# Performance work log

Hardware: AMD Instinct MI355X
Metric: run time of the kernel (lower is better)

Reference implementation:

```python
import jax, jax.numpy as jnp
import numpy as np

B, S, P, D, H = 2, 1024, 1024, 2048, 16
HD = D // H  # 128
T = P + S


def setup_inputs() -> dict:
    key = jax.random.key(0)
    ks = jax.random.split(key, 12)
    hidden_state = jax.random.normal(ks[0], (B, S, D), dtype=jnp.float32)
    past_key = jax.random.normal(ks[1], (B, H, P, HD), dtype=jnp.float32)
    past_value = jax.random.normal(ks[2], (B, H, P, HD), dtype=jnp.float32)
    # causal mask: query i sits at global position P+i; mask (1.0) keys j > P+i
    rows = P + jnp.arange(S)[:, None]
    cols = jnp.arange(T)[None, :]
    casual_mask = (cols > rows).astype(jnp.float32)[None, None]  # [1,1,S,T]
    # pad mask: mask out the last 128 key positions
    pad_mask = jnp.zeros((B, T), dtype=jnp.float32).at[:, T - 128:].set(1.0)
    init = lambda k, shp: (jax.random.normal(k, shp, dtype=jnp.float32) * 0.02)
    Wq, bq = init(ks[3], (D, D)), init(ks[4], (D,))
    Wk, bk = init(ks[5], (D, D)), init(ks[6], (D,))
    Wv, bv = init(ks[7], (D, D)), init(ks[8], (D,))
    Wo, bo = init(ks[9], (D, D)), init(ks[10], (D,))
    return dict(hidden_state=hidden_state, past_key=past_key, past_value=past_value,
                casual_mask=casual_mask, pad_mask=pad_mask,
                Wq=Wq, bq=bq, Wk=Wk, bk=bk, Wv=Wv, bv=bv, Wo=Wo, bo=bo)


def _split_heads(x):
    b, s, _ = x.shape
    return x.reshape(b, s, H, HD).transpose(0, 2, 1, 3)  # [B,H,S,HD]


def reference(hidden_state, past_key, past_value, casual_mask, pad_mask,
              Wq, bq, Wk, bk, Wv, bv, Wo, bo):
    q = _split_heads(jnp.einsum('bsd,ed->bse', hidden_state, Wq) + bq)
    k = _split_heads(jnp.einsum('bsd,ed->bse', hidden_state, Wk) + bk)
    v = _split_heads(jnp.einsum('bsd,ed->bse', hidden_state, Wv) + bv)
    k = jnp.concatenate([past_key, k], axis=2)   # [B,H,T,HD]
    v = jnp.concatenate([past_value, v], axis=2)
    scale = jnp.sqrt(jnp.float32(HD))
    scores = jnp.einsum('bhqd,bhkd->bhqk', q, k) / scale
    scores = scores + casual_mask * -1e9 + pad_mask[:, None, None, :] * -1e9
    probs = jax.nn.softmax(scores, axis=-1)
    out = jnp.einsum('bhqk,bhkd->bhqd', probs, v)
    out = out.transpose(0, 2, 1, 3).reshape(hidden_state.shape[0], -1, D)
    output = jnp.einsum('bsd,ed->bse', out, Wo) + bo
    # use_cache=True in original returns (output, (k, v)); return flat tuple
    return output, k, v
```

## Files before the change

kernel.cpp:

```cpp
#include <hip/hip_runtime.h>
#include <stdint.h>

typedef unsigned short u16t;
using bf16x8 = __attribute__((ext_vector_type(8))) short;
using f32x4  = __attribute__((ext_vector_type(4))) float;
using u16x8  = __attribute__((ext_vector_type(8))) unsigned short;
using fl4    = __attribute__((ext_vector_type(4))) float;

#define DEVI static __device__ __forceinline__

DEVI u16t f2bf(float x) {
    union { float f; unsigned u; } v; v.f = x;
    return (u16t)((v.u + 0x7fffu + ((v.u >> 16) & 1u)) >> 16);
}

#define GLL16(gp, lp) __builtin_amdgcn_global_load_lds( \
    (const __attribute__((address_space(1))) void*)(gp), \
    (__attribute__((address_space(3))) void*)(lp), 16, 0, 0)

DEVI f32x4 mfma16(bf16x8 a, bf16x8 b, f32x4 c) {
    return __builtin_amdgcn_mfma_f32_16x16x32_bf16(a, b, c, 0, 0, 0);
}

__global__ void k_f2bf(const float* __restrict__ src, u16t* __restrict__ dst) {
    size_t i = (size_t)blockIdx.x * blockDim.x + threadIdx.x;
    const fl4* s = (const fl4*)(src + i * 8);
    fl4 a = s[0], b = s[1];
    u16x8 o;
    o[0]=f2bf(a[0]); o[1]=f2bf(a[1]); o[2]=f2bf(a[2]); o[3]=f2bf(a[3]);
    o[4]=f2bf(b[0]); o[5]=f2bf(b[1]); o[6]=f2bf(b[2]); o[7]=f2bf(b[3]);
    *(u16x8*)(dst + i * 8) = o;
}

__global__ void k_copy_past(const float* __restrict__ src, u16t* __restrict__ dstb,
                            float* __restrict__ dstf) {
    size_t i = (size_t)blockIdx.x * blockDim.x + threadIdx.x;
    int bh = (int)(i >> 14);
    int r  = (int)(i & 16383);
    const fl4* s = (const fl4*)(src + i * 8);
    fl4 a = s[0], b = s[1];
    size_t dof = (size_t)bh * 262144 + (size_t)r * 8;
    *(fl4*)(dstf + dof) = a;
    *(fl4*)(dstf + dof + 4) = b;
    u16x8 o;
    o[0]=f2bf(a[0]); o[1]=f2bf(a[1]); o[2]=f2bf(a[2]); o[3]=f2bf(a[3]);
    o[4]=f2bf(b[0]); o[5]=f2bf(b[1]); o[6]=f2bf(b[2]); o[7]=f2bf(b[3]);
    *(u16x8*)(dstb + dof) = o;
}

__global__ void k_transpose_v(const u16t* __restrict__ Vb, u16t* __restrict__ Vtb) {
    __shared__ u16t tile[64 * 72];
    int bh  = blockIdx.z;
    int t0  = blockIdx.x * 64;
    int hd0 = blockIdx.y * 64;
    int tid = threadIdx.x;
    #pragma unroll
    for (int p = 0; p < 2; ++p) {
        int c = tid + p * 256;
        int tl = c >> 3, c8 = (c & 7) * 8;
        u16x8 v = *(const u16x8*)(Vb + ((size_t)bh * 2048 + t0 + tl) * 128 + hd0 + c8);
        *(u16x8*)(tile + tl * 72 + c8) = v;
    }
    __syncthreads();
    #pragma unroll
    for (int p = 0; p < 2; ++p) {
        int c = tid + p * 256;
        int hl = c >> 3, t8 = (c & 7) * 8;
        u16x8 v;
        #pragma unroll
        for (int j = 0; j < 8; ++j) v[j] = tile[(t8 + j) * 72 + hl];
        *(u16x8*)(Vtb + ((size_t)bh * 128 + hd0 + hl) * 2048 + t0 + t8) = v;
    }
}

template <int EPI>
__global__ void k_gemm(const u16t* __restrict__ A, const u16t* __restrict__ B,
                       const float* __restrict__ b0, const float* __restrict__ b1,
                       const float* __restrict__ b2,
                       u16t* __restrict__ Qb, u16t* __restrict__ Kb, u16t* __restrict__ Vb,
                       float* __restrict__ kout, float* __restrict__ vout,
                       float* __restrict__ outF) {
    __shared__ u16t As[128 * 64];
    __shared__ u16t Bs[128 * 64];
    const int tid  = threadIdx.x;
    const int lane = tid & 63;
    const int w    = tid >> 6;
    const int wm = w >> 1, wn = w & 1;
    const int m0 = blockIdx.x * 128;
    const int n0 = blockIdx.y * 128;
    const int srow = lane >> 3;
    const int scol = (lane & 7) * 8;
    const int fr = lane & 15, fg = lane >> 4;

    f32x4 acc[4][4] = {};

    const u16t* Ag = A + (size_t)(m0 + srow) * 2048 + scol;
    const u16t* Bg = B + (size_t)(n0 + srow) * 2048 + scol;

    for (int k0 = 0; k0 < 2048; k0 += 64) {
        #pragma unroll
        for (int j = 0; j < 4; ++j) {
            int is = w * 4 + j;
            GLL16(Ag + (size_t)is * 8 * 2048 + k0, As + is * 512);
            GLL16(Bg + (size_t)is * 8 * 2048 + k0, Bs + is * 512);
        }
        __syncthreads();
        bf16x8 af[2][4], bfr[2][4];
        #pragma unroll
        for (int m = 0; m < 4; ++m) {
            af[0][m] = *(const bf16x8*)(As + (wm * 64 + m * 16 + fr) * 64 + fg * 8);
            af[1][m] = *(const bf16x8*)(As + (wm * 64 + m * 16 + fr) * 64 + 32 + fg * 8);
        }
        #pragma unroll
        for (int n = 0; n < 4; ++n) {
            bfr[0][n] = *(const bf16x8*)(Bs + (wn * 64 + n * 16 + fr) * 64 + fg * 8);
            bfr[1][n] = *(const bf16x8*)(Bs + (wn * 64 + n * 16 + fr) * 64 + 32 + fg * 8);
        }
        #pragma unroll
        for (int kk = 0; kk < 2; ++kk)
            #pragma unroll
            for (int m = 0; m < 4; ++m)
                #pragma unroll
                for (int n = 0; n < 4; ++n)
                    acc[m][n] = mfma16(af[kk][m], bfr[kk][n], acc[m][n]);
        __syncthreads();
    }

    if (EPI == 0) {
        #pragma unroll
        for (int n = 0; n < 4; ++n) {
            int c = n0 + wn * 64 + n * 16 + fr;
            float bias = b0[c];
            #pragma unroll
            for (int m = 0; m < 4; ++m) {
                int r = m0 + wm * 64 + m * 16 + fg * 4;
                #pragma unroll
                for (int rr = 0; rr < 4; ++rr)
                    outF[(size_t)(r + rr) * 2048 + c] = acc[m][n][rr] + bias;
            }
        }
    } else {
        int group = n0 >> 11;
        const float* bias = (group == 0) ? b0 : (group == 1 ? b1 : b2);
        #pragma unroll
        for (int n = 0; n < 4; ++n) {
            int c = n0 + wn * 64 + n * 16 + fr;
            int e = c & 2047;
            int h = e >> 7, hd = e & 127;
            float bv = bias[e];
            #pragma unroll
            for (int m = 0; m < 4; ++m) {
                int r = m0 + wm * 64 + m * 16 + fg * 4;
                #pragma unroll
                for (int rr = 0; rr < 4; ++rr) {
                    int rg = r + rr;
                    int b = rg >> 10, s = rg & 1023;
                    float v = acc[m][n][rr] + bv;
                    if (group == 0) {
                        Qb[(((size_t)b * 16 + h) * 1024 + s) * 128 + hd] = f2bf(v);
                    } else {
                        size_t idx = (((size_t)b * 16 + h) * 2048 + 1024 + s) * 128 + hd;
                        if (group == 1) { Kb[idx] = f2bf(v); kout[idx] = v; }
                        else            { Vb[idx] = f2bf(v); vout[idx] = v; }
                    }
                }
            }
        }
    }
}

__global__ void k_flash(const u16t* __restrict__ Qb, const u16t* __restrict__ Kb,
                        const u16t* __restrict__ Vtb, u16t* __restrict__ Ao) {
    __shared__ u16t Ks[64 * 128];
    __shared__ u16t Vs[128 * 64];
    __shared__ u16t Ps[4 * 16 * 64];
    const int tid = threadIdx.x;
    const int lane = tid & 63;
    const int w = tid >> 6;
    const int bh = blockIdx.y;
    const int q0 = blockIdx.x * 64;
    const int fr = lane & 15, fg = lane >> 4;

    bf16x8 qf[4];
    {
        const u16t* qp = Qb + ((size_t)bh * 1024 + q0 + w * 16 + fr) * 128 + fg * 8;
        #pragma unroll
        for (int kk = 0; kk < 4; ++kk) qf[kk] = *(const bf16x8*)(qp + kk * 32);
    }

    f32x4 acc[8] = {};
    float m_r[4], l_r[4];
    #pragma unroll
    for (int rr = 0; rr < 4; ++rr) { m_r[rr] = -1e30f; l_r[rr] = 0.0f; }

    const int ntiles = min((1024 + q0 + 63) / 64 + 1, 30);

    const int krow_s = lane >> 4;
    const int koff_s = (lane & 15) * 8;
    const int vrow_s = lane >> 3;
    const int voff_s = (lane & 7) * 8;
    const int wqbase = 1024 + q0 + w * 16 + fg * 4;

    const u16t* Kg = Kb  + (size_t)bh * 262144;
    const u16t* Vg = Vtb + (size_t)bh * 262144;

    for (int t = 0; t < ntiles; ++t) {
        const int j0 = t * 64;
        #pragma unroll
        for (int j = 0; j < 4; ++j) {
            int is = w * 4 + j;
            int kr = is * 4 + krow_s;
            GLL16(Kg + (size_t)(j0 + kr) * 128 + (koff_s ^ ((kr & 7) << 3)), Ks + is * 512);
            int vr = is * 8 + vrow_s;
            GLL16(Vg + (size_t)vr * 2048 + j0 + (voff_s ^ ((vr & 7) << 3)), Vs + is * 512);
        }
        __syncthreads();

        f32x4 sc[4] = {};
        #pragma unroll
        for (int n = 0; n < 4; ++n) {
            int krow = n * 16 + fr;
            int sw = (krow & 7) << 3;
            #pragma unroll
            for (int kk = 0; kk < 4; ++kk) {
                bf16x8 kf = *(const bf16x8*)(Ks + krow * 128 + ((kk * 32 + fg * 8) ^ sw));
                sc[n] = mfma16(qf[kk], kf, sc[n]);
            }
        }

        const float scale = 0.08838834764831845f;
        float pv[4][4];
        float mt[4] = {-3e30f, -3e30f, -3e30f, -3e30f};
        if (j0 + 63 > 1024 + q0 + w * 16) {
            #pragma unroll
            for (int n = 0; n < 4; ++n) {
                int jcol = j0 + n * 16 + fr;
                #pragma unroll
                for (int rr = 0; rr < 4; ++rr) {
                    float v = sc[n][rr] * scale;
                    if (jcol > wqbase + rr) v = -3e30f;
                    pv[n][rr] = v;
                    mt[rr] = fmaxf(mt[rr], v);
                }
            }
        } else {
            #pragma unroll
            for (int n = 0; n < 4; ++n)
                #pragma unroll
                for (int rr = 0; rr < 4; ++rr) {
                    float v = sc[n][rr] * scale;
                    pv[n][rr] = v;
                    mt[rr] = fmaxf(mt[rr], v);
                }
        }

        #pragma unroll
        for (int rr = 0; rr < 4; ++rr) {
            float m = mt[rr];
            m = fmaxf(m, __shfl_xor(m, 1));
            m = fmaxf(m, __shfl_xor(m, 2));
            m = fmaxf(m, __shfl_xor(m, 4));
            m = fmaxf(m, __shfl_xor(m, 8));
            mt[rr] = m;
        }
        float cf[4], mn[4], ls[4];
        #pragma unroll
        for (int rr = 0; rr < 4; ++rr) {
            mn[rr] = fmaxf(m_r[rr], mt[rr]);
            cf[rr] = exp2f((m_r[rr] - mn[rr]) * 1.4426950408889634f);
            m_r[rr] = mn[rr];
            ls[rr] = 0.0f;
        }
        u16t* pw = Ps + w * 1024;
        #pragma unroll
        for (int n = 0; n < 4; ++n) {
            #pragma unroll
            for (int rr = 0; rr < 4; ++rr) {
                float p = exp2f((pv[n][rr] - mn[rr]) * 1.4426950408889634f);
                ls[rr] += p;
                int prow = fg * 4 + rr;
                pw[prow * 64 + ((n * 16 + fr) ^ ((prow & 7) << 3))] = f2bf(p);
            }
        }
        #pragma unroll
        for (int rr = 0; rr < 4; ++rr) {
            float s = ls[rr];
            s += __shfl_xor(s, 1);
            s += __shfl_xor(s, 2);
            s += __shfl_xor(s, 4);
            s += __shfl_xor(s, 8);
            l_r[rr] = l_r[rr] * cf[rr] + s;
        }
        #pragma unroll
        for (int cg = 0; cg < 8; ++cg)
            #pragma unroll
            for (int rr = 0; rr < 4; ++rr)
                acc[cg][rr] *= cf[rr];

        const int psw = (fr & 7) << 3;
        #pragma unroll
        for (int kk = 0; kk < 2; ++kk) {
            bf16x8 pa = *(const bf16x8*)(Ps + w * 1024 + fr * 64 + ((fg * 8 + kk * 32) ^ psw));
            #pragma unroll
            for (int cg = 0; cg < 8; ++cg) {
                int vrow = cg * 16 + fr;
                bf16x8 vf = *(const bf16x8*)(Vs + vrow * 64 + ((fg * 8 + kk * 32) ^ ((vrow & 7) << 3)));
                acc[cg] = mfma16(pa, vf, acc[cg]);
            }
        }
        __syncthreads();
    }

    float inv[4];
    #pragma unroll
    for (int rr = 0; rr < 4; ++rr) inv[rr] = 1.0f / l_r[rr];
    const int b = bh >> 4, h = bh & 15;
    const int sbase = q0 + w * 16 + fg * 4;
    #pragma unroll
    for (int cg = 0; cg < 8; ++cg) {
        #pragma unroll
        for (int rr = 0; rr < 4; ++rr) {
            size_t idx = ((size_t)b * 1024 + sbase + rr) * 2048 + h * 128 + cg * 16 + fr;
            Ao[idx] = f2bf(acc[cg][rr] * inv[rr]);
        }
    }
}

extern "C" void kernel_launch(void* const* d_in, const int* in_sizes, int n_in,
                              void* d_out, int out_size, void* d_ws, size_t ws_size,
                              hipStream_t stream) {
    const float* hidden = (const float*)d_in[0];
    const float* pkey   = (const float*)d_in[1];
    const float* pval   = (const float*)d_in[2];
    const float* Wq = (const float*)d_in[5];
    const float* bq = (const float*)d_in[6];
    const float* Wk = (const float*)d_in[7];
    const float* bk = (const float*)d_in[8];
    const float* Wv = (const float*)d_in[9];
    const float* bv = (const float*)d_in[10];
    const float* Wo = (const float*)d_in[11];
    const float* bo = (const float*)d_in[12];

    float* outp = (float*)d_out;
    float* kout = outp + 4194304;
    float* vout = outp + 12582912;

    char* ws = (char*)d_ws;
    u16t* Xb  = (u16t*)(ws);
    u16t* Wb  = (u16t*)(ws + (size_t)8  * 1048576);
    u16t* Qb  = (u16t*)(ws + (size_t)40 * 1048576);
    u16t* Kb  = (u16t*)(ws + (size_t)48 * 1048576);
    u16t* Vb  = (u16t*)(ws + (size_t)64 * 1048576);
    u16t* Vtb = (u16t*)(ws + (size_t)80 * 1048576);
    u16t* Ao  = Xb;
    if (ws_size < (size_t)96 * 1048576) return;

    k_f2bf<<<2048, 256, 0, stream>>>(hidden, Xb);
    k_f2bf<<<2048, 256, 0, stream>>>(Wq, Wb);
    k_f2bf<<<2048, 256, 0, stream>>>(Wk, Wb + 4194304);
    k_f2bf<<<2048, 256, 0, stream>>>(Wv, Wb + 8388608);
    k_f2bf<<<2048, 256, 0, stream>>>(Wo, Wb + 12582912);
    k_copy_past<<<2048, 256, 0, stream>>>(pkey, Kb, kout);
    k_copy_past<<<2048, 256, 0, stream>>>(pval, Vb, vout);
    k_gemm<1><<<dim3(16, 48), 256, 0, stream>>>(Xb, Wb, bq, bk, bv,
                                                Qb, Kb, Vb, kout, vout, nullptr);
    k_transpose_v<<<dim3(32, 2, 32), 256, 0, stream>>>(Vb, Vtb);
    k_flash<<<dim3(16, 32), 256, 0, stream>>>(Qb, Kb, Vtb, Ao);
    k_gemm<0><<<dim3(16, 16), 256, 0, stream>>>(Ao, Wb + 12582912, bo, nullptr, nullptr,
                                                nullptr, nullptr, nullptr, nullptr, nullptr, outp);
}
```

Measured before the change: 465.8 us.

## Double-buffer flash K/V tiles, keep P in registers, merge conversion launches

The flash kernel now double-buffers K and V tiles in LDS, prefetching the next tile while computing the current one. It also computes S transposed so P can be packed into MFMA A-operands with cvt_pk_bf16 and lane shuffles, skipping the LDS round trip for P. The grid is swapped so blocks of the same head are launched together, and the five f32-to-bf16 launches and two past-copy launches are merged into one launch each. The risks are the extra LDS for double buffering lowering occupancy, and correctness of the new swizzle and shuffle permutation.

```diff
diff --git a/kernel.cpp b/kernel.cpp
--- a/kernel.cpp
+++ b/kernel.cpp
@@ -5,6 +5,7 @@
 using bf16x8 = __attribute__((ext_vector_type(8))) short;
 using f32x4  = __attribute__((ext_vector_type(4))) float;
 using u16x8  = __attribute__((ext_vector_type(8))) unsigned short;
+using u32x4  = __attribute__((ext_vector_type(4))) unsigned int;
 using fl4    = __attribute__((ext_vector_type(4))) float;
 
 #define DEVI static __device__ __forceinline__
@@ -22,7 +23,22 @@
     return __builtin_amdgcn_mfma_f32_16x16x32_bf16(a, b, c, 0, 0, 0);
 }
 
-__global__ void k_f2bf(const float* __restrict__ src, u16t* __restrict__ dst) {
+DEVI unsigned cvt_pk_bf16(float lo, float hi) {
+    unsigned r;
+    asm("v_cvt_pk_bf16_f32 %0, %1, %2" : "=v"(r) : "v"(lo), "v"(hi));
+    return r;
+}
+
+__global__ void k_f2bf5(const float* __restrict__ h,  const float* __restrict__ wq,
+                        const float* __restrict__ wk, const float* __restrict__ wv,
+                        const float* __restrict__ wo, u16t* __restrict__ xb,
+                        u16t* __restrict__ wb) {
+    const float* src = h;  u16t* dst = xb;
+    int which = blockIdx.y;
+    if      (which == 1) { src = wq; dst = wb; }
+    else if (which == 2) { src = wk; dst = wb + 4194304; }
+    else if (which == 3) { src = wv; dst = wb + 8388608; }
+    else if (which == 4) { src = wo; dst = wb + 12582912; }
     size_t i = (size_t)blockIdx.x * blockDim.x + threadIdx.x;
     const fl4* s = (const fl4*)(src + i * 8);
     fl4 a = s[0], b = s[1];
@@ -32,8 +48,11 @@
     *(u16x8*)(dst + i * 8) = o;
 }
 
-__global__ void k_copy_past(const float* __restrict__ src, u16t* __restrict__ dstb,
-                            float* __restrict__ dstf) {
+__global__ void k_copy_past2(const float* __restrict__ pk, const float* __restrict__ pv,
+                             u16t* __restrict__ Kb, u16t* __restrict__ Vb,
+                             float* __restrict__ kout, float* __restrict__ vout) {
+    const float* src = pk; u16t* dstb = Kb; float* dstf = kout;
+    if (blockIdx.y == 1) { src = pv; dstb = Vb; dstf = vout; }
     size_t i = (size_t)blockIdx.x * blockDim.x + threadIdx.x;
     int bh = (int)(i >> 14);
     int r  = (int)(i & 16383);
@@ -171,14 +190,13 @@
 
 __global__ void k_flash(const u16t* __restrict__ Qb, const u16t* __restrict__ Kb,
                         const u16t* __restrict__ Vtb, u16t* __restrict__ Ao) {
-    __shared__ u16t Ks[64 * 128];
-    __shared__ u16t Vs[128 * 64];
-    __shared__ u16t Ps[4 * 16 * 64];
+    __shared__ u16t Ks[2][64 * 128];
+    __shared__ u16t Vs[2][128 * 64];
     const int tid = threadIdx.x;
     const int lane = tid & 63;
     const int w = tid >> 6;
-    const int bh = blockIdx.y;
-    const int q0 = blockIdx.x * 64;
+    const int bh = blockIdx.x;
+    const int q0 = blockIdx.y * 64;
     const int fr = lane & 15, fg = lane >> 4;
 
     bf16x8 qf[4];
@@ -189,131 +207,154 @@
     }
 
     f32x4 acc[8] = {};
-    float m_r[4], l_r[4];
-    #pragma unroll
-    for (int rr = 0; rr < 4; ++rr) { m_r[rr] = -1e30f; l_r[rr] = 0.0f; }
+    float m_r = -1e30f, l_r = 0.0f;
 
     const int ntiles = min((1024 + q0 + 63) / 64 + 1, 30);
 
     const int krow_s = lane >> 4;
     const int koff_s = (lane & 15) * 8;
     const int vrow_s = lane >> 3;
-    const int voff_s = (lane & 7) * 8;
-    const int wqbase = 1024 + q0 + w * 16 + fg * 4;
+    const int vc = (lane & 7) ^ (lane >> 3);
+    const int vperm8 = ((vc & 4) | ((vc & 1) << 1) | ((vc >> 1) & 1)) * 8;
+    const int qpos = 1024 + q0 + w * 16 + fr;
 
     const u16t* Kg = Kb  + (size_t)bh * 262144;
     const u16t* Vg = Vtb + (size_t)bh * 262144;
 
+#define STAGE(tt, bb) do {                                                        \
+    int j0s = (tt) * 64;                                                          \
+    _Pragma("unroll")                                                             \
+    for (int j = 0; j < 4; ++j) {                                                 \
+        int is = w * 4 + j;                                                       \
+        int kr = is * 4 + krow_s;                                                 \
+        GLL16(Kg + (size_t)(j0s + kr) * 128 + (koff_s ^ ((kr & 7) << 3)),         \
+              &Ks[bb][is * 512]);                                                 \
+        int vr = is * 8 + vrow_s;                                                 \
+        GLL16(Vg + (size_t)vr * 2048 + j0s + vperm8, &Vs[bb][is * 512]);          \
+    }                                                                             \
+} while (0)
+
+    int cur = 0;
+    STAGE(0, 0);
+    __syncthreads();
+
+    const float scale = 0.08838834764831845f;
+    const float L2E = 1.4426950408889634f;
+
     for (int t = 0; t < ntiles; ++t) {
+        if (t + 1 < ntiles) STAGE(t + 1, cur ^ 1);
         const int j0 = t * 64;
-        #pragma unroll
-        for (int j = 0; j < 4; ++j) {
-            int is = w * 4 + j;
-            int kr = is * 4 + krow_s;
-            GLL16(Kg + (size_t)(j0 + kr) * 128 + (koff_s ^ ((kr & 7) << 3)), Ks + is * 512);
-            int vr = is * 8 + vrow_s;
-            GLL16(Vg + (size_t)vr * 2048 + j0 + (voff_s ^ ((vr & 7) << 3)), Vs + is * 512);
-        }
-        __syncthreads();
+        const u16t* kb = &Ks[cur][0];
+        const u16t* vb = &Vs[cur][0];
 
         f32x4 sc[4] = {};
         #pragma unroll
-        for (int n = 0; n < 4; ++n) {
-            int krow = n * 16 + fr;
+        for (int kt = 0; kt < 4; ++kt) {
+            int krow = kt * 16 + fr;
             int sw = (krow & 7) << 3;
             #pragma unroll
             for (int kk = 0; kk < 4; ++kk) {
-                bf16x8 kf = *(const bf16x8*)(Ks + krow * 128 + ((kk * 32 + fg * 8) ^ sw));
-                sc[n] = mfma16(qf[kk], kf, sc[n]);
+                bf16x8 kf = *(const bf16x8*)(kb + krow * 128 + ((kk * 32 + fg * 8) ^ sw));
+                sc[kt] = mfma16(kf, qf[kk], sc[kt]);
             }
         }
 
-        const float scale = 0.08838834764831845f;
-        float pv[4][4];
-        float mt[4] = {-3e30f, -3e30f, -3e30f, -3e30f};
+        float pp[4][4];
+        float mt = -3e30f;
         if (j0 + 63 > 1024 + q0 + w * 16) {
             #pragma unroll
-            for (int n = 0; n < 4; ++n) {
-                int jcol = j0 + n * 16 + fr;
+            for (int kt = 0; kt < 4; ++kt)
                 #pragma unroll
                 for (int rr = 0; rr < 4; ++rr) {
-                    float v = sc[n][rr] * scale;
-                    if (jcol > wqbase + rr) v = -3e30f;
-                    pv[n][rr] = v;
-                    mt[rr] = fmaxf(mt[rr], v);
+                    float v = sc[kt][rr] * scale;
+                    int jk = j0 + kt * 16 + fg * 4 + rr;
+                    if (jk > qpos) v = -3e30f;
+                    pp[kt][rr] = v;
+                    mt = fmaxf(mt, v);
                 }
-            }
         } else {
             #pragma unroll
-            for (int n = 0; n < 4; ++n)
+            for (int kt = 0; kt < 4; ++kt)
                 #pragma unroll
                 for (int rr = 0; rr < 4; ++rr) {
-                    float v = sc[n][rr] * scale;
-                    pv[n][rr] = v;
-                    mt[rr] = fmaxf(mt[rr], v);
+                    float v = sc[kt][rr] * scale;
+                    pp[kt][rr] = v;
+                    mt = fmaxf(mt, v);
                 }
         }
-
-        #pragma unroll
-        for (int rr = 0; rr < 4; ++rr) {
-            float m = mt[rr];
-            m = fmaxf(m, __shfl_xor(m, 1));
-            m = fmaxf(m, __shfl_xor(m, 2));
-            m = fmaxf(m, __shfl_xor(m, 4));
-            m = fmaxf(m, __shfl_xor(m, 8));
-            mt[rr] = m;
-        }
-        float cf[4], mn[4], ls[4];
-        #pragma unroll
-        for (int rr = 0; rr < 4; ++rr) {
-            mn[rr] = fmaxf(m_r[rr], mt[rr]);
-            cf[rr] = exp2f((m_r[rr] - mn[rr]) * 1.4426950408889634f);
-            m_r[rr] = mn[rr];
-            ls[rr] = 0.0f;
-        }
-        u16t* pw = Ps + w * 1024;
-        #pragma unroll
-        for (int n = 0; n < 4; ++n) {
+        mt = fmaxf(mt, __shfl_xor(mt, 16));
+        mt = fmaxf(mt, __shfl_xor(mt, 32));
+        float mn = fmaxf(m_r, mt);
+        float cf = exp2f((m_r - mn) * L2E);
+        m_r = mn;
+        float ls = 0.0f;
+        #pragma unroll
+        for (int kt = 0; kt < 4; ++kt)
             #pragma unroll
             for (int rr = 0; rr < 4; ++rr) {
-                float p = exp2f((pv[n][rr] - mn[rr]) * 1.4426950408889634f);
-                ls[rr] += p;
-                int prow = fg * 4 + rr;
-                pw[prow * 64 + ((n * 16 + fr) ^ ((prow & 7) << 3))] = f2bf(p);
+                float p = exp2f((pp[kt][rr] - mn) * L2E);
+                pp[kt][rr] = p;
+                ls += p;
             }
-        }
-        #pragma unroll
-        for (int rr = 0; rr < 4; ++rr) {
-            float s = ls[rr];
-            s += __shfl_xor(s, 1);
-            s += __shfl_xor(s, 2);
-            s += __shfl_xor(s, 4);
-            s += __shfl_xor(s, 8);
-            l_r[rr] = l_r[rr] * cf[rr] + s;
-        }
+        ls += __shfl_xor(ls, 16);
+        ls += __shfl_xor(ls, 32);
+        l_r = l_r * cf + ls;
+
+        unsigned wp[4][2];
+        #pragma unroll
+        for (int kt = 0; kt < 4; ++kt) {
+            wp[kt][0] = cvt_pk_bf16(pp[kt][0], pp[kt][1]);
+            wp[kt][1] = cvt_pk_bf16(pp[kt][2], pp[kt][3]);
+        }
+        const bool fodd = (fg & 1) != 0;
+        unsigned X0 = fodd ? wp[0][0] : wp[1][0];
+        unsigned X1 = fodd ? wp[0][1] : wp[1][1];
+        unsigned X2 = fodd ? wp[2][0] : wp[3][0];
+        unsigned X3 = fodd ? wp[2][1] : wp[3][1];
+        unsigned Y0 = (unsigned)__shfl_xor((int)X0, 16);
+        unsigned Y1 = (unsigned)__shfl_xor((int)X1, 16);
+        unsigned Y2 = (unsigned)__shfl_xor((int)X2, 16);
+        unsigned Y3 = (unsigned)__shfl_xor((int)X3, 16);
+
+        float cfo[4];
+        #pragma unroll
+        for (int rr = 0; rr < 4; ++rr) cfo[rr] = __shfl(cf, fg * 4 + rr);
         #pragma unroll
         for (int cg = 0; cg < 8; ++cg)
             #pragma unroll
             for (int rr = 0; rr < 4; ++rr)
-                acc[cg][rr] *= cf[rr];
-
-        const int psw = (fr & 7) << 3;
+                acc[cg][rr] *= cfo[rr];
+
+        u32x4 a0v, a1v;
+        if (!fodd) {
+            a0v[0] = wp[0][0]; a0v[1] = wp[0][1]; a0v[2] = Y0; a0v[3] = Y1;
+            a1v[0] = wp[2][0]; a1v[1] = wp[2][1]; a1v[2] = Y2; a1v[3] = Y3;
+        } else {
+            a0v[0] = Y0; a0v[1] = Y1; a0v[2] = wp[1][0]; a0v[3] = wp[1][1];
+            a1v[0] = Y2; a1v[1] = Y3; a1v[2] = wp[3][0]; a1v[3] = wp[3][1];
+        }
+        bf16x8 pa0 = __builtin_bit_cast(bf16x8, a0v);
+        bf16x8 pa1 = __builtin_bit_cast(bf16x8, a1v);
+
         #pragma unroll
         for (int kk = 0; kk < 2; ++kk) {
-            bf16x8 pa = *(const bf16x8*)(Ps + w * 1024 + fr * 64 + ((fg * 8 + kk * 32) ^ psw));
+            bf16x8 pa = kk ? pa1 : pa0;
             #pragma unroll
             for (int cg = 0; cg < 8; ++cg) {
                 int vrow = cg * 16 + fr;
-                bf16x8 vf = *(const bf16x8*)(Vs + vrow * 64 + ((fg * 8 + kk * 32) ^ ((vrow & 7) << 3)));
+                bf16x8 vf = *(const bf16x8*)(vb + vrow * 64 +
+                                             ((fg * 8 + kk * 32) ^ ((vrow & 7) << 3)));
                 acc[cg] = mfma16(pa, vf, acc[cg]);
             }
         }
         __syncthreads();
-    }
-
-    float inv[4];
+        cur ^= 1;
+    }
+#undef STAGE
+
+    float linv[4];
     #pragma unroll
-    for (int rr = 0; rr < 4; ++rr) inv[rr] = 1.0f / l_r[rr];
+    for (int rr = 0; rr < 4; ++rr) linv[rr] = 1.0f / __shfl(l_r, fg * 4 + rr);
     const int b = bh >> 4, h = bh & 15;
     const int sbase = q0 + w * 16 + fg * 4;
     #pragma unroll
@@ -321,7 +362,7 @@
         #pragma unroll
         for (int rr = 0; rr < 4; ++rr) {
             size_t idx = ((size_t)b * 1024 + sbase + rr) * 2048 + h * 128 + cg * 16 + fr;
-            Ao[idx] = f2bf(acc[cg][rr] * inv[rr]);
+            Ao[idx] = f2bf(acc[cg][rr] * linv[rr]);
         }
     }
 }
@@ -355,17 +396,12 @@
     u16t* Ao  = Xb;
     if (ws_size < (size_t)96 * 1048576) return;
 
-    k_f2bf<<<2048, 256, 0, stream>>>(hidden, Xb);
-    k_f2bf<<<2048, 256, 0, stream>>>(Wq, Wb);
-    k_f2bf<<<2048, 256, 0, stream>>>(Wk, Wb + 4194304);
-    k_f2bf<<<2048, 256, 0, stream>>>(Wv, Wb + 8388608);
-    k_f2bf<<<2048, 256, 0, stream>>>(Wo, Wb + 12582912);
-    k_copy_past<<<2048, 256, 0, stream>>>(pkey, Kb, kout);
-    k_copy_past<<<2048, 256, 0, stream>>>(pval, Vb, vout);
+    k_f2bf5<<<dim3(2048, 5), 256, 0, stream>>>(hidden, Wq, Wk, Wv, Wo, Xb, Wb);
+    k_copy_past2<<<dim3(2048, 2), 256, 0, stream>>>(pkey, pval, Kb, Vb, kout, vout);
     k_gemm<1><<<dim3(16, 48), 256, 0, stream>>>(Xb, Wb, bq, bk, bv,
                                                 Qb, Kb, Vb, kout, vout, nullptr);
     k_transpose_v<<<dim3(32, 2, 32), 256, 0, stream>>>(Vb, Vtb);
-    k_flash<<<dim3(16, 32), 256, 0, stream>>>(Qb, Kb, Vtb, Ao);
+    k_flash<<<dim3(32, 16), 256, 0, stream>>>(Qb, Kb, Vtb, Ao);
     k_gemm<0><<<dim3(16, 16), 256, 0, stream>>>(Ao, Wb + 12582912, bo, nullptr, nullptr,
                                                 nullptr, nullptr, nullptr, nullptr, nullptr, outp);
 }
```

Result: faster. 387.4 us (-16.8%).
